# Optimization experiments

Hardware: AMD Instinct MI355X
Metric: run time of the kernel (lower is better)

## Reference

```python
import jax, jax.numpy as jnp
import numpy as np

NEG_BIG = -9.0e15  # matches torch's -9000000000000000.0 mask fill
ALPHA = 0.2        # leakyrelu negative slope


def setup_inputs() -> dict:
    key = jax.random.key(0)
    k1, k2, k3, k4, k5 = jax.random.split(key, 5)
    N, F_in, F_out = 4096, 512, 64
    stdv = 1.0 / np.sqrt(F_out)
    x = jax.random.normal(k1, (N, F_in), dtype=jnp.float32)
    adj = jax.random.randint(k2, (N, N), 0, 2, dtype=jnp.int32)
    W = jax.random.uniform(k3, (F_in, F_out), dtype=jnp.float32, minval=-stdv, maxval=stdv)
    a = jax.random.normal(k4, (2 * F_out, 1), dtype=jnp.float32) * 0.1
    bias = jax.random.uniform(k5, (F_out,), dtype=jnp.float32, minval=-stdv, maxval=stdv)
    return {"x": x, "adj": adj, "W": W, "a": a, "bias": bias}


def _gat_forward(x, adj, W, a, bias):
    N = x.shape[0]
    F_out = W.shape[1]
    h = x @ W  # (N, F)
    a1 = a[:F_out, 0]   # weights hitting the first concat half
    a2 = a[F_out:, 0]   # weights hitting the second concat half
    # First half: row k=i*N+j of the concat holds h_j  ->  e1[j] = h_j . a1
    e1 = h @ a1  # (N,)
    # Second half of this repo's concat is NOT h_i; exact index algebra:
    # second[k=i*N+j, r] = h[(r*N+i)//F, (((r*N+i)%F)*N + j) % F]
    # Since it depends on j only via j % F, build table T[i, t] (t = j % F).
    r = jnp.arange(F_out)[:, None]          # (F, 1)
    i = jnp.arange(N)[None, :]              # (1, N)
    m = r * N + i                           # (F, N)
    p = m // F_out                          # row index into h
    s0 = m % F_out
    t = jnp.arange(F_out)                   # (F,)
    col = (s0[..., None] * N + t) % F_out   # (F, N, F) column index into h
    vals = h[p[..., None], col]             # (F, N, F)
    T = jnp.einsum('r,rit->it', a2, vals)   # (N, F)
    j = jnp.arange(N)
    e2 = T[:, j % F_out]                    # (N, N) second-half contribution
    e = e1[None, :] + e2                    # (N, N) pre-activation scores
    e = jnp.where(e > 0, e, ALPHA * e)      # LeakyReLU(0.2)
    e = jnp.where(adj > 0, e, NEG_BIG)      # mask non-edges
    att = jax.nn.softmax(e, axis=1)         # row-wise softmax (dropout = eval identity)
    out = jax.nn.relu(att @ h) + bias       # relu BEFORE bias add, as in source
    return out


def reference(x, adj, W, a, bias):
    return _gat_forward(x, adj, W, a, bias)
```

## Files before the change

### kernel.cpp

```cpp
#include <hip/hip_runtime.h>
#include <math.h>

#define N_NODES 4096
#define F_IN    512
#define F_OUT   64
#define ALPHA   0.2f
#define NPART   16

typedef _Float16 half8 __attribute__((ext_vector_type(8)));
typedef _Float16 half4 __attribute__((ext_vector_type(4)));
typedef float    floatx4 __attribute__((ext_vector_type(4)));

__global__ __launch_bounds__(256) void k_prep(const float* __restrict__ W,
                                              _Float16* __restrict__ WT) {
    int idx = blockIdx.x * 256 + threadIdx.x;
    int t = idx >> 9;
    int k = idx & 511;
    WT[idx] = (_Float16)W[k * F_OUT + t];
}

__global__ __launch_bounds__(256) void k_hW(const float* __restrict__ x,
                                            const _Float16* __restrict__ WT,
                                            const float* __restrict__ a,
                                            float* __restrict__ h,
                                            _Float16* __restrict__ hT,
                                            float* __restrict__ e1) {
    __shared__ float red[4][16][64];
    int tid  = threadIdx.x;
    int lane = tid & 63;
    int w    = tid >> 6;
    int i0   = blockIdx.x * 16;
    int n    = lane & 15;
    int quad = lane >> 4;

    floatx4 acc[4] = {{0,0,0,0},{0,0,0,0},{0,0,0,0},{0,0,0,0}};

    const float* xr = x + (size_t)(i0 + n) * F_IN + w * 128 + quad * 8;
    const _Float16* wb = WT + w * 128 + quad * 8;
#pragma unroll
    for (int kk = 0; kk < 128; kk += 32) {
        float4 x0 = *(const float4*)(xr + kk);
        float4 x1 = *(const float4*)(xr + kk + 4);
        half8 af = {(_Float16)x0.x, (_Float16)x0.y, (_Float16)x0.z, (_Float16)x0.w,
                    (_Float16)x1.x, (_Float16)x1.y, (_Float16)x1.z, (_Float16)x1.w};
#pragma unroll
        for (int g = 0; g < 4; ++g) {
            half8 bf = *(const half8*)(wb + (size_t)(g * 16 + n) * F_IN + kk);
            acc[g] = __builtin_amdgcn_mfma_f32_16x16x32_f16(af, bf, acc[g], 0, 0, 0);
        }
    }
#pragma unroll
    for (int g = 0; g < 4; ++g)
#pragma unroll
        for (int r = 0; r < 4; ++r)
            red[w][g * 4 + r][lane] = acc[g][r];
    __syncthreads();
    if (w != 0) return;
#pragma unroll
    for (int g = 0; g < 4; ++g)
#pragma unroll
        for (int r = 0; r < 4; ++r)
            acc[g][r] = red[0][g * 4 + r][lane] + red[1][g * 4 + r][lane] +
                        red[2][g * 4 + r][lane] + red[3][g * 4 + r][lane];
#pragma unroll
    for (int g = 0; g < 4; ++g) {
        half4 hv;
#pragma unroll
        for (int r = 0; r < 4; ++r) {
            h[(size_t)(i0 + quad * 4 + r) * F_OUT + g * 16 + n] = acc[g][r];
            hv[r] = (_Float16)acc[g][r];
        }
        *(half4*)(hT + (size_t)(g * 16 + n) * N_NODES + i0 + quad * 4) = hv;
    }
    float a1v[4];
#pragma unroll
    for (int g = 0; g < 4; ++g) a1v[g] = a[g * 16 + n];
#pragma unroll
    for (int r = 0; r < 4; ++r) {
        float v = acc[0][r] * a1v[0] + acc[1][r] * a1v[1] + acc[2][r] * a1v[2] + acc[3][r] * a1v[3];
        v += __shfl_xor(v, 1, 64);
        v += __shfl_xor(v, 2, 64);
        v += __shfl_xor(v, 4, 64);
        v += __shfl_xor(v, 8, 64);
        if (n == 0) e1[i0 + quad * 4 + r] = v;
    }
}

__global__ __launch_bounds__(256) void k_TqP(const float* __restrict__ h,
                                             const float* __restrict__ a,
                                             const float* __restrict__ e1,
                                             _Float16* __restrict__ P) {
    __shared__ float part[4][64];
    __shared__ float TqS[64];
    int q = blockIdx.x;
    int tid = threadIdx.x;
    int t = tid & 63;
    int rp = tid >> 6;
    const float* a2 = a + F_OUT;
    float s = 0.f;
#pragma unroll
    for (int rr = 0; rr < 16; ++rr) {
        int r = rp * 16 + rr;
        s += a2[r] * h[(size_t)(r * 64 + q) * F_OUT + t];
    }
    part[rp][t] = s;
    __syncthreads();
    if (tid < 64) TqS[tid] = part[0][tid] + part[1][tid] + part[2][tid] + part[3][tid];
    __syncthreads();
#pragma unroll
    for (int it = 0; it < 4; ++it) {
        int j = (it * 256 + tid) * 4;
        float4 ev = *(const float4*)(e1 + j);
        float4 tv = *(const float4*)(TqS + (j & 63));
        float e[4] = {ev.x + tv.x, ev.y + tv.y, ev.z + tv.z, ev.w + tv.w};
        half4 pv;
#pragma unroll
        for (int r = 0; r < 4; ++r) {
            float xx = e[r] > 0.f ? e[r] : ALPHA * e[r];
            pv[r] = (_Float16)__expf(xx);
        }
        *(half4*)(P + (size_t)q * N_NODES + j) = pv;
    }
}

__global__ __launch_bounds__(256, 4) void k_main(const int* __restrict__ adj,
                                                 const _Float16* __restrict__ P,
                                                 const _Float16* __restrict__ hT,
                                                 float* __restrict__ out_part,
                                                 float* __restrict__ den_part) {
    int tid  = threadIdx.x;
    int lane = tid & 63;
    int w    = tid >> 6;
    int waveId = blockIdx.x * 4 + w;
    int g   = waveId >> 4;
    int s   = waveId & 15;
    int i0  = g * 16;
    int q   = i0 >> 6;
    int n    = lane & 15;
    int quad = lane >> 4;
    int jbase = s * 256 + quad * 8;

    const int*      arow = adj + (size_t)(i0 + n) * N_NODES + jbase;
    const _Float16* prow = P + (size_t)q * N_NODES + jbase;
    const _Float16* hrow = hT + (size_t)n * N_NODES + jbase;

    int4 abuf[16];
#pragma unroll
    for (int c = 0; c < 8; ++c) {
        abuf[2 * c]     = *(const int4*)(arow + c * 32);
        abuf[2 * c + 1] = *(const int4*)(arow + c * 32 + 4);
    }
    __builtin_amdgcn_sched_barrier(0);

    floatx4 acc[4] = {{0,0,0,0},{0,0,0,0},{0,0,0,0},{0,0,0,0}};
    floatx4 accd = {0, 0, 0, 0};
    _Float16 one_h = (n == 0) ? (_Float16)1.0f : (_Float16)0.0f;
    half8 ones_f = {one_h, one_h, one_h, one_h, one_h, one_h, one_h, one_h};

#pragma unroll
    for (int c = 0; c < 8; ++c) {
        int joff = c * 32;
        int4 a0 = abuf[2 * c];
        int4 a1v = abuf[2 * c + 1];
        half8 pv = *(const half8*)(prow + joff);
        half8 af;
        af[0] = a0.x  > 0 ? pv[0] : (_Float16)0.f;
        af[1] = a0.y  > 0 ? pv[1] : (_Float16)0.f;
        af[2] = a0.z  > 0 ? pv[2] : (_Float16)0.f;
        af[3] = a0.w  > 0 ? pv[3] : (_Float16)0.f;
        af[4] = a1v.x > 0 ? pv[4] : (_Float16)0.f;
        af[5] = a1v.y > 0 ? pv[5] : (_Float16)0.f;
        af[6] = a1v.z > 0 ? pv[6] : (_Float16)0.f;
        af[7] = a1v.w > 0 ? pv[7] : (_Float16)0.f;
#pragma unroll
        for (int g4 = 0; g4 < 4; ++g4) {
            half8 bf = *(const half8*)(hrow + (size_t)g4 * 16 * N_NODES + joff);
            acc[g4] = __builtin_amdgcn_mfma_f32_16x16x32_f16(af, bf, acc[g4], 0, 0, 0);
        }
        accd = __builtin_amdgcn_mfma_f32_16x16x32_f16(af, ones_f, accd, 0, 0, 0);
    }
    float* op = out_part + ((size_t)s * N_NODES + i0) * F_OUT;
#pragma unroll
    for (int g4 = 0; g4 < 4; ++g4)
#pragma unroll
        for (int r = 0; r < 4; ++r)
            op[(quad * 4 + r) * F_OUT + g4 * 16 + n] = acc[g4][r];
    if (n == 0) {
#pragma unroll
        for (int r = 0; r < 4; ++r)
            den_part[s * N_NODES + i0 + quad * 4 + r] = accd[r];
    }
}

__global__ __launch_bounds__(256) void k_out(const float* __restrict__ out_part,
                                             const float* __restrict__ den_part,
                                             const float* __restrict__ bias,
                                             float* __restrict__ out) {
    int idx = blockIdx.x * 256 + threadIdx.x;
    int i = idx >> 6;
    int t = idx & 63;
    float sacc = 0.f, dacc = 0.f;
#pragma unroll
    for (int p = 0; p < NPART; ++p)
        sacc += out_part[(size_t)p * N_NODES * F_OUT + idx];
#pragma unroll
    for (int p = 0; p < NPART; ++p)
        dacc += den_part[p * N_NODES + i];
    float v = sacc / dacc;
    v = v > 0.f ? v : 0.f;
    out[idx] = v + bias[t];
}

extern "C" void kernel_launch(void* const* d_in, const int* in_sizes, int n_in,
                              void* d_out, int out_size, void* d_ws, size_t ws_size,
                              hipStream_t stream) {
    const float* x    = (const float*)d_in[0];
    const int*   adj  = (const int*)d_in[1];
    const float* W    = (const float*)d_in[2];
    const float* a    = (const float*)d_in[3];
    const float* bias = (const float*)d_in[4];
    float* out = (float*)d_out;

    char* ws = (char*)d_ws;
    float*    h        = (float*)ws;
    _Float16* hT       = (_Float16*)(ws + 1024 * 1024);
    float*    e1       = (float*)(ws + 1536 * 1024);
    _Float16* P        = (_Float16*)(ws + 1552 * 1024);
    _Float16* WT       = (_Float16*)(ws + 2064 * 1024);
    float*    out_part = (float*)(ws + 2128 * 1024);
    float*    den_part = (float*)(ws + (2128 + 16384) * 1024);

    k_prep<<<128, 256, 0, stream>>>(W, WT);
    k_hW  <<<256, 256, 0, stream>>>(x, WT, a, h, hT, e1);
    k_TqP <<<64, 256, 0, stream>>>(h, a, e1, P);
    k_main<<<1024, 256, 0, stream>>>(adj, P, hT, out_part, den_part);
    k_out <<<1024, 256, 0, stream>>>(out_part, den_part, bias, out);
}
```

Measured before the change: 139.1 us.

## Split j-range into 32 partitions, remap waves per block, vectorize reduction

Doubles the number of column partitions in the main attention-aggregation kernel (each wave handles 128 columns instead of 256) and remaps blocks so the four waves in a block share a column slice over consecutive row groups. P loads are hoisted alongside the adj loads. The final reduction kernel is vectorized to float4 over the larger partition count. More parallelism and memory-level concurrency in k_main come at the cost of twice the partial-sum traffic written and then reduced.

```diff
diff --git a/kernel.cpp b/kernel.cpp
--- a/kernel.cpp
+++ b/kernel.cpp
@@ -5,7 +5,7 @@
 #define F_IN    512
 #define F_OUT   64
 #define ALPHA   0.2f
-#define NPART   16
+#define NPART   32
 
 typedef _Float16 half8 __attribute__((ext_vector_type(8)));
 typedef _Float16 half4 __attribute__((ext_vector_type(4)));
@@ -131,26 +131,27 @@
     int tid  = threadIdx.x;
     int lane = tid & 63;
     int w    = tid >> 6;
-    int waveId = blockIdx.x * 4 + w;
-    int g   = waveId >> 4;
-    int s   = waveId & 15;
-    int i0  = g * 16;
-    int q   = i0 >> 6;
+    int b    = blockIdx.x;
+    int s    = b & 31;
+    int g    = (b >> 5) * 4 + w;
+    int i0   = g * 16;
+    int q    = i0 >> 6;
     int n    = lane & 15;
     int quad = lane >> 4;
-    int jbase = s * 256 + quad * 8;
+    int jbase = s * 128 + quad * 8;
 
     const int*      arow = adj + (size_t)(i0 + n) * N_NODES + jbase;
     const _Float16* prow = P + (size_t)q * N_NODES + jbase;
     const _Float16* hrow = hT + (size_t)n * N_NODES + jbase;
 
-    int4 abuf[16];
-#pragma unroll
-    for (int c = 0; c < 8; ++c) {
-        abuf[2 * c]     = *(const int4*)(arow + c * 32);
-        abuf[2 * c + 1] = *(const int4*)(arow + c * 32 + 4);
-    }
-    __builtin_amdgcn_sched_barrier(0);
+    int4 a0[4], a1[4];
+    half8 pv[4];
+#pragma unroll
+    for (int c = 0; c < 4; ++c) {
+        a0[c] = *(const int4*)(arow + c * 32);
+        a1[c] = *(const int4*)(arow + c * 32 + 4);
+        pv[c] = *(const half8*)(prow + c * 32);
+    }
 
     floatx4 acc[4] = {{0,0,0,0},{0,0,0,0},{0,0,0,0},{0,0,0,0}};
     floatx4 accd = {0, 0, 0, 0};
@@ -158,20 +159,17 @@
     half8 ones_f = {one_h, one_h, one_h, one_h, one_h, one_h, one_h, one_h};
 
 #pragma unroll
-    for (int c = 0; c < 8; ++c) {
+    for (int c = 0; c < 4; ++c) {
         int joff = c * 32;
-        int4 a0 = abuf[2 * c];
-        int4 a1v = abuf[2 * c + 1];
-        half8 pv = *(const half8*)(prow + joff);
         half8 af;
-        af[0] = a0.x  > 0 ? pv[0] : (_Float16)0.f;
-        af[1] = a0.y  > 0 ? pv[1] : (_Float16)0.f;
-        af[2] = a0.z  > 0 ? pv[2] : (_Float16)0.f;
-        af[3] = a0.w  > 0 ? pv[3] : (_Float16)0.f;
-        af[4] = a1v.x > 0 ? pv[4] : (_Float16)0.f;
-        af[5] = a1v.y > 0 ? pv[5] : (_Float16)0.f;
-        af[6] = a1v.z > 0 ? pv[6] : (_Float16)0.f;
-        af[7] = a1v.w > 0 ? pv[7] : (_Float16)0.f;
+        af[0] = a0[c].x > 0 ? pv[c][0] : (_Float16)0.f;
+        af[1] = a0[c].y > 0 ? pv[c][1] : (_Float16)0.f;
+        af[2] = a0[c].z > 0 ? pv[c][2] : (_Float16)0.f;
+        af[3] = a0[c].w > 0 ? pv[c][3] : (_Float16)0.f;
+        af[4] = a1[c].x > 0 ? pv[c][4] : (_Float16)0.f;
+        af[5] = a1[c].y > 0 ? pv[c][5] : (_Float16)0.f;
+        af[6] = a1[c].z > 0 ? pv[c][6] : (_Float16)0.f;
+        af[7] = a1[c].w > 0 ? pv[c][7] : (_Float16)0.f;
 #pragma unroll
         for (int g4 = 0; g4 < 4; ++g4) {
             half8 bf = *(const half8*)(hrow + (size_t)g4 * 16 * N_NODES + joff);
@@ -196,19 +194,25 @@
                                              const float* __restrict__ den_part,
                                              const float* __restrict__ bias,
                                              float* __restrict__ out) {
-    int idx = blockIdx.x * 256 + threadIdx.x;
-    int i = idx >> 6;
-    int t = idx & 63;
-    float sacc = 0.f, dacc = 0.f;
-#pragma unroll
-    for (int p = 0; p < NPART; ++p)
-        sacc += out_part[(size_t)p * N_NODES * F_OUT + idx];
-#pragma unroll
-    for (int p = 0; p < NPART; ++p)
+    int idx4 = blockIdx.x * 256 + threadIdx.x;
+    int base = idx4 * 4;
+    int i = base >> 6;
+    int t = base & 63;
+    float4 sacc = {0.f, 0.f, 0.f, 0.f};
+    float dacc = 0.f;
+#pragma unroll
+    for (int p = 0; p < NPART; ++p) {
+        float4 v = ((const float4*)(out_part + (size_t)p * N_NODES * F_OUT))[idx4];
+        sacc.x += v.x; sacc.y += v.y; sacc.z += v.z; sacc.w += v.w;
         dacc += den_part[p * N_NODES + i];
-    float v = sacc / dacc;
-    v = v > 0.f ? v : 0.f;
-    out[idx] = v + bias[t];
+    }
+    float4 bv = *(const float4*)(bias + t);
+    float4 o;
+    o.x = fmaxf(sacc.x / dacc, 0.f) + bv.x;
+    o.y = fmaxf(sacc.y / dacc, 0.f) + bv.y;
+    o.z = fmaxf(sacc.z / dacc, 0.f) + bv.z;
+    o.w = fmaxf(sacc.w / dacc, 0.f) + bv.w;
+    ((float4*)out)[idx4] = o;
 }
 
 extern "C" void kernel_launch(void* const* d_in, const int* in_sizes, int n_in,
@@ -228,11 +232,11 @@
     _Float16* P        = (_Float16*)(ws + 1552 * 1024);
     _Float16* WT       = (_Float16*)(ws + 2064 * 1024);
     float*    out_part = (float*)(ws + 2128 * 1024);
-    float*    den_part = (float*)(ws + (2128 + 16384) * 1024);
+    float*    den_part = (float*)(ws + (2128 + 32768) * 1024);
 
     k_prep<<<128, 256, 0, stream>>>(W, WT);
     k_hW  <<<256, 256, 0, stream>>>(x, WT, a, h, hT, e1);
     k_TqP <<<64, 256, 0, stream>>>(h, a, e1, P);
-    k_main<<<1024, 256, 0, stream>>>(adj, P, hT, out_part, den_part);
-    k_out <<<1024, 256, 0, stream>>>(out_part, den_part, bias, out);
-}
+    k_main<<<2048, 256, 0, stream>>>(adj, P, hT, out_part, den_part);
+    k_out <<<256, 256, 0, stream>>>(out_part, den_part, bias, out);
+}
```

New measurement: 139.7 us. No clear change (+0.4%).
